# Optimization experiments

Hardware: AMD Instinct MI355X
Metric: run time of the kernel (lower is better)

Reference implementation:

```python
import jax, jax.numpy as jnp
import numpy as np

B, C, H, W = 1, 64, 128, 128
HEADS, NWIN, TOPK = 8, 16, 4
EPS = 1e-6


def dwconv(x, w, b, pad):
    # x: NCHW, w: (C,1,k,k) depthwise conv weight
    y = jax.lax.conv_general_dilated(
        x, w, (1, 1), [(pad, pad), (pad, pad)],
        dimension_numbers=('NCHW', 'OIHW', 'NCHW'),
        feature_group_count=x.shape[1])
    return y + b[None, :, None, None]


def layernorm(x, g, b):
    m = x.mean(-1, keepdims=True)
    v = ((x - m) ** 2).mean(-1, keepdims=True)
    return (x - m) * jax.lax.rsqrt(v + EPS) * g + b


def drf_attn(x, qkv_w, qkv_b, wo_w, wo_b, lepe_w, lepe_b):
    # x: (B,H,W,C) NHWC, BiFormer-style top-k routed window attention
    Bb, Hh, Ww, Cc = x.shape
    h, w = Hh // NWIN, Ww // NWIN
    hw, p2 = h * w, NWIN * NWIN
    # window partition -> (B, p2, hw, C)
    xw = x.reshape(Bb, NWIN, h, NWIN, w, Cc).transpose(0, 1, 3, 2, 4, 5).reshape(Bb, p2, hw, Cc)
    qkv = xw @ qkv_w + qkv_b                       # (B,p2,hw,3C), qk_dim == dim
    q, kv = qkv[..., :Cc], qkv[..., Cc:]
    # window-level routing: per-window mean q/k
    q_win = q.mean(2)                              # (B,p2,C)
    k_win = kv[..., :Cc].mean(2)                   # (B,p2,C)
    logits = jnp.einsum('bpc,bqc->bpq', q_win, k_win)
    _, idx = jax.lax.top_k(logits, TOPK)           # (B,p2,TOPK) int32
    # gather top-k kv windows for each query window -> (B,p2,TOPK,hw,2C)
    kv_sel = jax.vmap(lambda kvb, ib: kvb[ib])(kv, idx)
    hd = Cc // HEADS
    k_sel = kv_sel[..., :Cc].reshape(Bb, p2, TOPK * hw, HEADS, hd).transpose(0, 1, 3, 2, 4)
    v_sel = kv_sel[..., Cc:].reshape(Bb, p2, TOPK * hw, HEADS, hd).transpose(0, 1, 3, 2, 4)
    q_h = q.reshape(Bb, p2, hw, HEADS, hd).transpose(0, 1, 3, 2, 4)
    scale = Cc ** -0.5                             # qk_dim ** -0.5 as in torch module
    attn = jax.nn.softmax(jnp.einsum('bpnqd,bpnkd->bpnqk', q_h * scale, k_sel), axis=-1)
    out = jnp.einsum('bpnqk,bpnkd->bpnqd', attn, v_sel)
    out = out.transpose(0, 1, 3, 2, 4).reshape(Bb, p2, hw, Cc)
    # un-window -> (B,H,W,C)
    out = out.reshape(Bb, NWIN, NWIN, h, w, Cc).transpose(0, 1, 3, 2, 4, 5).reshape(Bb, Hh, Ww, Cc)
    # LePE: depthwise 5x5 conv on full-image v
    v_full = kv[..., Cc:].reshape(Bb, NWIN, NWIN, h, w, Cc).transpose(0, 1, 3, 2, 4, 5).reshape(Bb, Hh, Ww, Cc)
    lepe = dwconv(v_full.transpose(0, 3, 1, 2), lepe_w, lepe_b, 2).transpose(0, 2, 3, 1)
    return (out + lepe) @ wo_w + wo_b


def setup_inputs() -> dict:
    key = jax.random.key(0)
    ks = jax.random.split(key, 8)
    s = lambda k, shape: jax.random.normal(k, shape, jnp.float32) * 0.02
    return {
        'x': jax.random.normal(ks[0], (B, C, H, W), jnp.float32),
        'pos_w': s(ks[1], (C, 1, 3, 3)), 'pos_b': jnp.zeros((C,), jnp.float32),
        'norm_g': jnp.ones((C,), jnp.float32), 'norm_b': jnp.zeros((C,), jnp.float32),
        'qkv_w': s(ks[2], (C, 3 * C)), 'qkv_b': jnp.zeros((3 * C,), jnp.float32),
        'wo_w': s(ks[3], (C, C)), 'wo_b': jnp.zeros((C,), jnp.float32),
        'lepe_w': s(ks[4], (C, 1, 5, 5)), 'lepe_b': jnp.zeros((C,), jnp.float32),
        'mlp_w1': s(ks[5], (C, 4 * C)), 'mlp_b1': jnp.zeros((4 * C,), jnp.float32),
        'mlp_w2': s(ks[6], (4 * C, C)), 'mlp_b2': jnp.zeros((C,), jnp.float32),
    }


def reference(x, pos_w, pos_b, norm_g, norm_b, qkv_w, qkv_b, wo_w, wo_b,
              lepe_w, lepe_b, mlp_w1, mlp_b1, mlp_w2, mlp_b2):
    x = x + dwconv(x, pos_w, pos_b, 1)             # dwconv pos-embed (NCHW)
    x = x.transpose(0, 2, 3, 1)                    # -> NHWC
    x = x + drf_attn(layernorm(x, norm_g, norm_b), qkv_w, qkv_b, wo_w, wo_b, lepe_w, lepe_b)
    y = layernorm(x, norm_g, norm_b)               # same LayerNorm weights reused
    y = jax.nn.gelu(y @ mlp_w1 + mlp_b1, approximate=False) @ mlp_w2 + mlp_b2
    x = x + y
    return x.transpose(0, 3, 1, 2)                 # -> NCHW
```

## Files before the change

### kernel.cpp

```cpp
#include <hip/hip_runtime.h>
#include <hip/hip_bf16.h>
#include <math.h>

#define HPIX 128
#define WPIX 128
#define NPIX (HPIX*WPIX)
#define CCH 64
#define P2 256
#define HWIN 64
#define LNS 36

__device__ __forceinline__ float waveReduceSum(float v){
  #pragma unroll
  for (int m = 32; m >= 1; m >>= 1) v += __shfl_xor(v, m);
  return v;
}

__device__ __forceinline__ float gelu_exact(float h){
  return 0.5f*h*(1.f + erff(h*0.70710678118654752f));
}

__global__ void k1_posconv(const float* __restrict__ x, const float* __restrict__ pw,
                           const float* __restrict__ pb, float* __restrict__ x1){
  int tid = threadIdx.x;
  int pl = tid & 63;
  int cl = tid >> 6;
  int pix0 = (blockIdx.x & 255) * 64;
  int cg   = (blockIdx.x >> 8);
  int c = cg*4 + cl;
  int pix = pix0 + pl;
  int y = pix >> 7, xx = pix & 127;
  const float* xc = x + c*NPIX;
  float acc = pb[c];
  #pragma unroll
  for (int dy=0; dy<3; dy++){
    int yy = y+dy-1; if ((unsigned)yy >= (unsigned)HPIX) continue;
    #pragma unroll
    for (int dx=0; dx<3; dx++){
      int x2 = xx+dx-1; if ((unsigned)x2 >= (unsigned)WPIX) continue;
      acc += pw[c*9 + dy*3 + dx] * xc[yy*WPIX + x2];
    }
  }
  __shared__ float lds[4][64];
  lds[cl][pl] = xc[pix] + acc;
  __syncthreads();
  int pp = tid >> 2, cc = tid & 3;
  x1[(pix0+pp)*CCH + cg*4 + cc] = lds[cc][pp];
}

__global__ void k2_ln_qkv(const float* __restrict__ x1,
                          const float* __restrict__ g, const float* __restrict__ bb,
                          const float* __restrict__ qw, const float* __restrict__ qb,
                          float* __restrict__ qkv){
  __shared__ float lnT[64][LNS];
  int tid = threadIdx.x, w = tid >> 6, lane = tid & 63;
  int pix0 = blockIdx.x * 32;
  #pragma unroll
  for (int i=0; i<8; i++){
    int pl = w*8 + i, pix = pix0 + pl;
    float v = x1[pix*CCH + lane];
    float mean = waveReduceSum(v) * (1.f/64.f);
    float d = v - mean;
    float var = waveReduceSum(d*d) * (1.f/64.f);
    lnT[lane][pl] = d * rsqrtf(var + 1e-6f) * g[lane] + bb[lane];
  }
  __syncthreads();
  int p0 = (tid & 7) * 4;
  int cg = tid >> 3;
  int j0 = cg * 6;
  float acc[4][6];
  #pragma unroll
  for (int i=0;i<4;i++)
    #pragma unroll
    for (int j=0;j<6;j++) acc[i][j] = qb[j0+j];
  #pragma unroll 4
  for (int k=0; k<64; k++){
    float4 a = *(const float4*)&lnT[k][p0];
    const float* wr = qw + k*192 + j0;
    float2 u0 = *(const float2*)(wr);
    float2 u1 = *(const float2*)(wr+2);
    float2 u2 = *(const float2*)(wr+4);
    float av[4] = {a.x, a.y, a.z, a.w};
    #pragma unroll
    for (int i=0;i<4;i++){
      acc[i][0] += av[i]*u0.x; acc[i][1] += av[i]*u0.y;
      acc[i][2] += av[i]*u1.x; acc[i][3] += av[i]*u1.y;
      acc[i][4] += av[i]*u2.x; acc[i][5] += av[i]*u2.y;
    }
  }
  int y = pix0 >> 7;
  #pragma unroll
  for (int i=0;i<4;i++){
    int pix = pix0 + p0 + i;
    int xx = pix & 127;
    int p = (y>>3)*16 + (xx>>3);
    int r = ((y&7)<<3) + (xx&7);
    float* o = qkv + (p*HWIN + r)*192 + j0;
    *(float2*)(o)     = make_float2(acc[i][0], acc[i][1]);
    *(float2*)(o + 2) = make_float2(acc[i][2], acc[i][3]);
    *(float2*)(o + 4) = make_float2(acc[i][4], acc[i][5]);
  }
}

__global__ void k3_winmean(const float* __restrict__ qkv,
                           float* __restrict__ qwin, float* __restrict__ kwinT){
  int p = blockIdx.x;
  int tid = threadIdx.x, rq = tid >> 6, c = tid & 63;
  float sq = 0.f, sk = 0.f;
  for (int r = rq*16; r < rq*16+16; r++){
    const float* row = qkv + (p*HWIN + r)*192;
    sq += row[c];
    sk += row[64 + c];
  }
  __shared__ float s1[4][64], s2[4][64];
  s1[rq][c] = sq; s2[rq][c] = sk;
  __syncthreads();
  if (tid < 64){
    qwin[p*64 + c]   = (s1[0][c]+s1[1][c]+s1[2][c]+s1[3][c])*(1.f/64.f);
    kwinT[c*P2 + p]  = (s2[0][c]+s2[1][c]+s2[2][c]+s2[3][c])*(1.f/64.f);
  }
}

__global__ void k4_topk(const float* __restrict__ qwin, const float* __restrict__ kwinT,
                        int* __restrict__ idx){
  int p = blockIdx.x, t = threadIdx.x;
  int w = t >> 6, lane = t & 63;
  __shared__ float qs[64];
  __shared__ float lg[P2];
  __shared__ float wv[4]; __shared__ int wi[4];
  if (t < 64) qs[t] = qwin[p*64 + t];
  __syncthreads();
  float acc = 0.f;
  #pragma unroll 8
  for (int c=0; c<64; c++) acc += qs[c] * kwinT[c*P2 + t];
  lg[t] = acc;
  __syncthreads();
  for (int j=0; j<4; j++){
    float v = lg[t]; int i = t;
    #pragma unroll
    for (int m=32; m>=1; m>>=1){
      float ov = __shfl_xor(v, m); int oi = __shfl_xor(i, m);
      if (ov > v || (ov == v && oi < i)){ v = ov; i = oi; }
    }
    if (lane == 0){ wv[w] = v; wi[w] = i; }
    __syncthreads();
    if (t == 0){
      float bv = wv[0]; int bi = wi[0];
      #pragma unroll
      for (int u=1; u<4; u++)
        if (wv[u] > bv || (wv[u] == bv && wi[u] < bi)){ bv = wv[u]; bi = wi[u]; }
      idx[p*4 + j] = bi;
      lg[bi] = -1e30f;
    }
    __syncthreads();
  }
}

__global__ void k5_attn(const float* __restrict__ qkv, const int* __restrict__ idx,
                        float* __restrict__ attnout){
  int p = blockIdx.x >> 3, n = blockIdx.x & 7;
  int tid = threadIdx.x, w = tid >> 6, lane = tid & 63;
  __shared__ float Ks[256][8];
  __shared__ float Vs[256][8];
  __shared__ int wsel[4];
  __shared__ float ps[4][64][9];
  if (tid < 4) wsel[tid] = idx[p*4 + tid];
  __syncthreads();
  int cb = n*8;
  for (int u = tid; u < 512; u += 256){
    int k = u >> 1, h = u & 1;
    const float* row = qkv + (wsel[k>>6]*HWIN + (k&63))*192;
    *(float4*)&Ks[k][h*4] = *(const float4*)(row + 64  + cb + h*4);
    *(float4*)&Vs[k][h*4] = *(const float4*)(row + 128 + cb + h*4);
  }
  __syncthreads();
  const float* qrow = qkv + (p*HWIN + lane)*192 + cb;
  float q[8];
  #pragma unroll
  for (int d=0; d<8; d++) q[d] = qrow[d] * 0.125f;
  float l = 0.f, acc[8];
  #pragma unroll
  for (int d=0; d<8; d++) acc[d] = 0.f;
  #pragma unroll 4
  for (int k = w*64; k < w*64+64; k++){
    float4 ka = *(float4*)&Ks[k][0];
    float4 kb = *(float4*)&Ks[k][4];
    float s = q[0]*ka.x + q[1]*ka.y + q[2]*ka.z + q[3]*ka.w
            + q[4]*kb.x + q[5]*kb.y + q[6]*kb.z + q[7]*kb.w;
    float e = __expf(s);
    l += e;
    float4 va = *(float4*)&Vs[k][0];
    float4 vb = *(float4*)&Vs[k][4];
    acc[0]+=e*va.x; acc[1]+=e*va.y; acc[2]+=e*va.z; acc[3]+=e*va.w;
    acc[4]+=e*vb.x; acc[5]+=e*vb.y; acc[6]+=e*vb.z; acc[7]+=e*vb.w;
  }
  ps[w][lane][8] = l;
  #pragma unroll
  for (int d=0; d<8; d++) ps[w][lane][d] = acc[d];
  __syncthreads();
  if (w == 0){
    float L = 0.f, o[8];
    #pragma unroll
    for (int d=0; d<8; d++) o[d] = 0.f;
    #pragma unroll
    for (int u=0; u<4; u++){
      L += ps[u][lane][8];
      #pragma unroll
      for (int d=0; d<8; d++) o[d] += ps[u][lane][d];
    }
    float inv = 1.f / L;
    int yy = (p>>4)*8 + (lane>>3), xx = (p&15)*8 + (lane&7);
    float* orow = attnout + (yy*WPIX + xx)*CCH + cb;
    #pragma unroll
    for (int d=0; d<8; d++) orow[d] = o[d]*inv;
  }
}

__global__ void k6_lepe_wo(const float* __restrict__ attnout, const float* __restrict__ qkv,
                           const float* __restrict__ lw, const float* __restrict__ lb,
                           const float* __restrict__ ww, const float* __restrict__ wb,
                           float* __restrict__ x1){
  __shared__ float tT[64][LNS];
  int tid = threadIdx.x, w = tid >> 6, lane = tid & 63;
  int pix0 = blockIdx.x * 32;
  for (int i=0; i<8; i++){
    int pl = w*8 + i, pix = pix0 + pl;
    int y = pix >> 7, xx = pix & 127;
    float acc = lb[lane];
    #pragma unroll
    for (int dy=0; dy<5; dy++){
      int yy = y+dy-2; if ((unsigned)yy >= (unsigned)HPIX) continue;
      #pragma unroll
      for (int dx=0; dx<5; dx++){
        int x2 = xx+dx-2; if ((unsigned)x2 >= (unsigned)WPIX) continue;
        int pp = (yy>>3)*16 + (x2>>3), rr = ((yy&7)<<3) + (x2&7);
        acc += lw[lane*25 + dy*5 + dx] * qkv[(pp*HWIN + rr)*192 + 128 + lane];
      }
    }
    tT[lane][pl] = attnout[pix*CCH + lane] + acc;
  }
  __syncthreads();
  int p0 = (tid & 7) * 4;
  int cg = tid >> 3;
  int j0 = cg * 2;
  float a0[4], a1[4];
  #pragma unroll
  for (int i=0;i<4;i++){ a0[i] = wb[j0]; a1[i] = wb[j0+1]; }
  #pragma unroll 4
  for (int k=0; k<64; k++){
    float4 a = *(const float4*)&tT[k][p0];
    float2 u = *(const float2*)(ww + k*64 + j0);
    a0[0]+=a.x*u.x; a1[0]+=a.x*u.y;
    a0[1]+=a.y*u.x; a1[1]+=a.y*u.y;
    a0[2]+=a.z*u.x; a1[2]+=a.z*u.y;
    a0[3]+=a.w*u.x; a1[3]+=a.w*u.y;
  }
  #pragma unroll
  for (int i=0;i<4;i++){
    int pix = pix0 + p0 + i;
    float* xb = x1 + pix*CCH + j0;
    float2 r = *(float2*)xb;
    r.x += a0[i]; r.y += a1[i];
    *(float2*)xb = r;
  }
}

__global__ void k7_mlp_out(const float* __restrict__ x2,
                           const float* __restrict__ g, const float* __restrict__ bb,
                           const float* __restrict__ w1, const float* __restrict__ b1,
                           const float* __restrict__ w2, const float* __restrict__ b2,
                           float* __restrict__ out){
  __shared__ float lnT[64][LNS];
  __shared__ float hidT[256][LNS];
  int tid = threadIdx.x, w = tid >> 6, lane = tid & 63;
  int pix0 = blockIdx.x * 32;
  #pragma unroll
  for (int i=0; i<8; i++){
    int pl = w*8 + i, pix = pix0 + pl;
    float v = x2[pix*CCH + lane];
    float mean = waveReduceSum(v) * (1.f/64.f);
    float d = v - mean;
    float var = waveReduceSum(d*d) * (1.f/64.f);
    lnT[lane][pl] = d * rsqrtf(var + 1e-6f) * g[lane] + bb[lane];
  }
  __syncthreads();
  int p0 = (tid & 7) * 4;
  int cg = tid >> 3;
  {
    int j0 = cg * 8;
    float acc[4][8];
    #pragma unroll
    for (int i=0;i<4;i++)
      #pragma unroll
      for (int j=0;j<8;j++) acc[i][j] = b1[j0+j];
    #pragma unroll 2
    for (int k=0; k<64; k++){
      float4 a = *(const float4*)&lnT[k][p0];
      const float* wr = w1 + k*256 + j0;
      float4 u0 = *(const float4*)(wr);
      float4 u1 = *(const float4*)(wr + 4);
      float av[4] = {a.x, a.y, a.z, a.w};
      #pragma unroll
      for (int i=0;i<4;i++){
        acc[i][0]+=av[i]*u0.x; acc[i][1]+=av[i]*u0.y;
        acc[i][2]+=av[i]*u0.z; acc[i][3]+=av[i]*u0.w;
        acc[i][4]+=av[i]*u1.x; acc[i][5]+=av[i]*u1.y;
        acc[i][6]+=av[i]*u1.z; acc[i][7]+=av[i]*u1.w;
      }
    }
    #pragma unroll
    for (int j=0;j<8;j++){
      float4 hv;
      hv.x = gelu_exact(acc[0][j]);
      hv.y = gelu_exact(acc[1][j]);
      hv.z = gelu_exact(acc[2][j]);
      hv.w = gelu_exact(acc[3][j]);
      *(float4*)&hidT[j0+j][p0] = hv;
    }
  }
  __syncthreads();
  {
    int j0 = cg * 2;
    float a0[4], a1[4];
    #pragma unroll
    for (int i=0;i<4;i++){ a0[i] = b2[j0]; a1[i] = b2[j0+1]; }
    #pragma unroll 4
    for (int k=0; k<256; k++){
      float4 a = *(const float4*)&hidT[k][p0];
      float2 u = *(const float2*)(w2 + k*64 + j0);
      a0[0]+=a.x*u.x; a1[0]+=a.x*u.y;
      a0[1]+=a.y*u.x; a1[1]+=a.y*u.y;
      a0[2]+=a.z*u.x; a1[2]+=a.z*u.y;
      a0[3]+=a.w*u.x; a1[3]+=a.w*u.y;
    }
    float4 o0, o1;
    float* r0 = &o0.x; float* r1 = &o1.x;
    #pragma unroll
    for (int i=0;i<4;i++){
      int pix = pix0 + p0 + i;
      r0[i] = x2[pix*CCH + j0]     + a0[i];
      r1[i] = x2[pix*CCH + j0 + 1] + a1[i];
    }
    *(float4*)&out[j0*NPIX + pix0 + p0]     = o0;
    *(float4*)&out[(j0+1)*NPIX + pix0 + p0] = o1;
  }
}

extern "C" void kernel_launch(void* const* d_in, const int* in_sizes, int n_in,
                              void* d_out, int out_size, void* d_ws, size_t ws_size,
                              hipStream_t stream) {
  (void)in_sizes; (void)n_in; (void)out_size; (void)ws_size;
  const float* x      = (const float*)d_in[0];
  const float* pos_w  = (const float*)d_in[1];
  const float* pos_b  = (const float*)d_in[2];
  const float* norm_g = (const float*)d_in[3];
  const float* norm_b = (const float*)d_in[4];
  const float* qkv_w  = (const float*)d_in[5];
  const float* qkv_b  = (const float*)d_in[6];
  const float* wo_w   = (const float*)d_in[7];
  const float* wo_b   = (const float*)d_in[8];
  const float* lepe_w = (const float*)d_in[9];
  const float* lepe_b = (const float*)d_in[10];
  const float* mlp_w1 = (const float*)d_in[11];
  const float* mlp_b1 = (const float*)d_in[12];
  const float* mlp_w2 = (const float*)d_in[13];
  const float* mlp_b2 = (const float*)d_in[14];
  float* out = (float*)d_out;

  char* ws = (char*)d_ws;
  float* x1      = (float*)(ws);
  float* qkv     = (float*)(ws + (4u<<20));
  float* qwin    = (float*)(ws + (16u<<20));
  float* kwinT   = (float*)(ws + (16u<<20) + (64u<<10));
  int*   idx     = (int*)  (ws + (16u<<20) + (128u<<10));
  float* attnout = (float*)(ws + (17u<<20));

  hipLaunchKernelGGL(k1_posconv, dim3(4096), dim3(256), 0, stream, x, pos_w, pos_b, x1);
  hipLaunchKernelGGL(k2_ln_qkv,  dim3(512),  dim3(256), 0, stream, x1, norm_g, norm_b, qkv_w, qkv_b, qkv);
  hipLaunchKernelGGL(k3_winmean, dim3(256),  dim3(256), 0, stream, qkv, qwin, kwinT);
  hipLaunchKernelGGL(k4_topk,    dim3(256),  dim3(256), 0, stream, qwin, kwinT, idx);
  hipLaunchKernelGGL(k5_attn,    dim3(2048), dim3(256), 0, stream, qkv, idx, attnout);
  hipLaunchKernelGGL(k6_lepe_wo, dim3(512),  dim3(256), 0, stream, attnout, qkv, lepe_w, lepe_b, wo_w, wo_b, x1);
  hipLaunchKernelGGL(k7_mlp_out, dim3(512),  dim3(256), 0, stream, x1, norm_g, norm_b, mlp_w1, mlp_b1, mlp_w2, mlp_b2, out);
}
```

Baseline: 213.3 us.

## Retile QKV GEMM to 64-pixel blocks and split-K the MLP down-projection

The LN+QKV kernel now handles 64 pixels per block with 512 threads and a wider LDS tile. Its inner loop is unrolled by two k steps so more weight loads are in flight at once. In the MLP kernel, the second GEMM is split along K across the four waves, each computing a 4x8 tile, and the partials are reduced through reused shared memory before the residual add and NCHW store. The aim is more work per thread and better weight reuse in the down-projection, at the cost of an extra LDS reduction pass and less coalesced output stores.

Result: faster. 201.9 us (-5.3%).

```diff
diff --git a/kernel.cpp b/kernel.cpp
--- a/kernel.cpp
+++ b/kernel.cpp
@@ -9,6 +9,7 @@
 #define P2 256
 #define HWIN 64
 #define LNS 36
+#define LNS2 68
 
 __device__ __forceinline__ float waveReduceSum(float v){
   #pragma unroll
@@ -52,9 +53,9 @@
                           const float* __restrict__ g, const float* __restrict__ bb,
                           const float* __restrict__ qw, const float* __restrict__ qb,
                           float* __restrict__ qkv){
-  __shared__ float lnT[64][LNS];
+  __shared__ __align__(16) float lnT[64][LNS2];
   int tid = threadIdx.x, w = tid >> 6, lane = tid & 63;
-  int pix0 = blockIdx.x * 32;
+  int pix0 = blockIdx.x * 64;
   #pragma unroll
   for (int i=0; i<8; i++){
     int pl = w*8 + i, pix = pix0 + pl;
@@ -65,36 +66,47 @@
     lnT[lane][pl] = d * rsqrtf(var + 1e-6f) * g[lane] + bb[lane];
   }
   __syncthreads();
-  int p0 = (tid & 7) * 4;
-  int cg = tid >> 3;
+  int p0 = (tid & 15) * 4;
+  int cg = tid >> 4;
   int j0 = cg * 6;
   float acc[4][6];
   #pragma unroll
   for (int i=0;i<4;i++)
     #pragma unroll
     for (int j=0;j<6;j++) acc[i][j] = qb[j0+j];
-  #pragma unroll 4
-  for (int k=0; k<64; k++){
-    float4 a = *(const float4*)&lnT[k][p0];
-    const float* wr = qw + k*192 + j0;
-    float2 u0 = *(const float2*)(wr);
-    float2 u1 = *(const float2*)(wr+2);
-    float2 u2 = *(const float2*)(wr+4);
-    float av[4] = {a.x, a.y, a.z, a.w};
+  for (int k0=0; k0<64; k0+=2){
+    float4 a0 = *(const float4*)&lnT[k0][p0];
+    float4 a1 = *(const float4*)&lnT[k0+1][p0];
+    const float* wr0 = qw + k0*192 + j0;
+    const float* wr1 = wr0 + 192;
+    float2 u00 = *(const float2*)(wr0);
+    float2 u01 = *(const float2*)(wr0+2);
+    float2 u02 = *(const float2*)(wr0+4);
+    float2 u10 = *(const float2*)(wr1);
+    float2 u11 = *(const float2*)(wr1+2);
+    float2 u12 = *(const float2*)(wr1+4);
+    float a0v[4] = {a0.x,a0.y,a0.z,a0.w};
+    float a1v[4] = {a1.x,a1.y,a1.z,a1.w};
     #pragma unroll
     for (int i=0;i<4;i++){
-      acc[i][0] += av[i]*u0.x; acc[i][1] += av[i]*u0.y;
-      acc[i][2] += av[i]*u1.x; acc[i][3] += av[i]*u1.y;
-      acc[i][4] += av[i]*u2.x; acc[i][5] += av[i]*u2.y;
+      acc[i][0]+=a0v[i]*u00.x; acc[i][1]+=a0v[i]*u00.y;
+      acc[i][2]+=a0v[i]*u01.x; acc[i][3]+=a0v[i]*u01.y;
+      acc[i][4]+=a0v[i]*u02.x; acc[i][5]+=a0v[i]*u02.y;
+    }
+    #pragma unroll
+    for (int i=0;i<4;i++){
+      acc[i][0]+=a1v[i]*u10.x; acc[i][1]+=a1v[i]*u10.y;
+      acc[i][2]+=a1v[i]*u11.x; acc[i][3]+=a1v[i]*u11.y;
+      acc[i][4]+=a1v[i]*u12.x; acc[i][5]+=a1v[i]*u12.y;
     }
   }
   int y = pix0 >> 7;
+  int pb_row = (y>>3)*16, rrow = (y&7)<<3, xbase = pix0 & 127;
   #pragma unroll
   for (int i=0;i<4;i++){
-    int pix = pix0 + p0 + i;
-    int xx = pix & 127;
-    int p = (y>>3)*16 + (xx>>3);
-    int r = ((y&7)<<3) + (xx&7);
+    int xx = xbase + p0 + i;
+    int p = pb_row + (xx>>3);
+    int r = rrow + (xx&7);
     float* o = qkv + (p*HWIN + r)*192 + j0;
     *(float2*)(o)     = make_float2(acc[i][0], acc[i][1]);
     *(float2*)(o + 2) = make_float2(acc[i][2], acc[i][3]);
@@ -270,8 +282,10 @@
                            const float* __restrict__ w1, const float* __restrict__ b1,
                            const float* __restrict__ w2, const float* __restrict__ b2,
                            float* __restrict__ out){
-  __shared__ float lnT[64][LNS];
-  __shared__ float hidT[256][LNS];
+  __shared__ __align__(16) float smem[11520];
+  float (*lnT)[LNS]  = (float(*)[LNS])smem;
+  float (*hidT)[LNS] = (float(*)[LNS])(smem + 64*LNS);
+  float* red = smem;
   int tid = threadIdx.x, w = tid >> 6, lane = tid & 63;
   int pix0 = blockIdx.x * 32;
   #pragma unroll
@@ -284,28 +298,38 @@
     lnT[lane][pl] = d * rsqrtf(var + 1e-6f) * g[lane] + bb[lane];
   }
   __syncthreads();
-  int p0 = (tid & 7) * 4;
-  int cg = tid >> 3;
   {
-    int j0 = cg * 8;
+    int p0 = (tid & 7) * 4;
+    int j0 = (tid >> 3) * 8;
     float acc[4][8];
     #pragma unroll
     for (int i=0;i<4;i++)
       #pragma unroll
       for (int j=0;j<8;j++) acc[i][j] = b1[j0+j];
-    #pragma unroll 2
-    for (int k=0; k<64; k++){
-      float4 a = *(const float4*)&lnT[k][p0];
-      const float* wr = w1 + k*256 + j0;
-      float4 u0 = *(const float4*)(wr);
-      float4 u1 = *(const float4*)(wr + 4);
-      float av[4] = {a.x, a.y, a.z, a.w};
+    for (int k0=0; k0<64; k0+=2){
+      float4 a0 = *(const float4*)&lnT[k0][p0];
+      float4 a1 = *(const float4*)&lnT[k0+1][p0];
+      const float* wr0 = w1 + k0*256 + j0;
+      const float* wr1 = wr0 + 256;
+      float4 u00 = *(const float4*)(wr0);
+      float4 u01 = *(const float4*)(wr0+4);
+      float4 u10 = *(const float4*)(wr1);
+      float4 u11 = *(const float4*)(wr1+4);
+      float a0v[4] = {a0.x,a0.y,a0.z,a0.w};
+      float a1v[4] = {a1.x,a1.y,a1.z,a1.w};
       #pragma unroll
       for (int i=0;i<4;i++){
-        acc[i][0]+=av[i]*u0.x; acc[i][1]+=av[i]*u0.y;
-        acc[i][2]+=av[i]*u0.z; acc[i][3]+=av[i]*u0.w;
-        acc[i][4]+=av[i]*u1.x; acc[i][5]+=av[i]*u1.y;
-        acc[i][6]+=av[i]*u1.z; acc[i][7]+=av[i]*u1.w;
+        acc[i][0]+=a0v[i]*u00.x; acc[i][1]+=a0v[i]*u00.y;
+        acc[i][2]+=a0v[i]*u00.z; acc[i][3]+=a0v[i]*u00.w;
+        acc[i][4]+=a0v[i]*u01.x; acc[i][5]+=a0v[i]*u01.y;
+        acc[i][6]+=a0v[i]*u01.z; acc[i][7]+=a0v[i]*u01.w;
+      }
+      #pragma unroll
+      for (int i=0;i<4;i++){
+        acc[i][0]+=a1v[i]*u10.x; acc[i][1]+=a1v[i]*u10.y;
+        acc[i][2]+=a1v[i]*u10.z; acc[i][3]+=a1v[i]*u10.w;
+        acc[i][4]+=a1v[i]*u11.x; acc[i][5]+=a1v[i]*u11.y;
+        acc[i][6]+=a1v[i]*u11.z; acc[i][7]+=a1v[i]*u11.w;
       }
     }
     #pragma unroll
@@ -319,30 +343,76 @@
     }
   }
   __syncthreads();
+  float acc2[4][8];
   {
-    int j0 = cg * 2;
-    float a0[4], a1[4];
-    #pragma unroll
-    for (int i=0;i<4;i++){ a0[i] = b2[j0]; a1[i] = b2[j0+1]; }
-    #pragma unroll 4
-    for (int k=0; k<256; k++){
-      float4 a = *(const float4*)&hidT[k][p0];
-      float2 u = *(const float2*)(w2 + k*64 + j0);
-      a0[0]+=a.x*u.x; a1[0]+=a.x*u.y;
-      a0[1]+=a.y*u.x; a1[1]+=a.y*u.y;
-      a0[2]+=a.z*u.x; a1[2]+=a.z*u.y;
-      a0[3]+=a.w*u.x; a1[3]+=a.w*u.y;
-    }
-    float4 o0, o1;
-    float* r0 = &o0.x; float* r1 = &o1.x;
-    #pragma unroll
-    for (int i=0;i<4;i++){
-      int pix = pix0 + p0 + i;
-      r0[i] = x2[pix*CCH + j0]     + a0[i];
-      r1[i] = x2[pix*CCH + j0 + 1] + a1[i];
-    }
-    *(float4*)&out[j0*NPIX + pix0 + p0]     = o0;
-    *(float4*)&out[(j0+1)*NPIX + pix0 + p0] = o1;
+    int p0 = (lane & 7) * 4;
+    int c0 = (lane >> 3) * 8;
+    #pragma unroll
+    for (int i=0;i<4;i++)
+      #pragma unroll
+      for (int j=0;j<8;j++) acc2[i][j] = 0.f;
+    int kbase = w*64;
+    for (int k0=0; k0<64; k0+=2){
+      int k = kbase + k0;
+      float4 a0 = *(const float4*)&hidT[k][p0];
+      float4 a1 = *(const float4*)&hidT[k+1][p0];
+      const float* wr0 = w2 + k*64 + c0;
+      const float* wr1 = wr0 + 64;
+      float4 u00 = *(const float4*)(wr0);
+      float4 u01 = *(const float4*)(wr0+4);
+      float4 u10 = *(const float4*)(wr1);
+      float4 u11 = *(const float4*)(wr1+4);
+      float a0v[4] = {a0.x,a0.y,a0.z,a0.w};
+      float a1v[4] = {a1.x,a1.y,a1.z,a1.w};
+      #pragma unroll
+      for (int i=0;i<4;i++){
+        acc2[i][0]+=a0v[i]*u00.x; acc2[i][1]+=a0v[i]*u00.y;
+        acc2[i][2]+=a0v[i]*u00.z; acc2[i][3]+=a0v[i]*u00.w;
+        acc2[i][4]+=a0v[i]*u01.x; acc2[i][5]+=a0v[i]*u01.y;
+        acc2[i][6]+=a0v[i]*u01.z; acc2[i][7]+=a0v[i]*u01.w;
+      }
+      #pragma unroll
+      for (int i=0;i<4;i++){
+        acc2[i][0]+=a1v[i]*u10.x; acc2[i][1]+=a1v[i]*u10.y;
+        acc2[i][2]+=a1v[i]*u10.z; acc2[i][3]+=a1v[i]*u10.w;
+        acc2[i][4]+=a1v[i]*u11.x; acc2[i][5]+=a1v[i]*u11.y;
+        acc2[i][6]+=a1v[i]*u11.z; acc2[i][7]+=a1v[i]*u11.w;
+      }
+    }
+  }
+  __syncthreads();
+  #pragma unroll
+  for (int t=0; t<16; t++){
+    int s = 2*t, i = s >> 3, j = s & 7;
+    *(float2*)&red[tid*34 + s] = make_float2(acc2[i][j], acc2[i][j+1]);
+  }
+  __syncthreads();
+  {
+    int lane_r = tid & 63, ir = tid >> 6;
+    int pg = lane_r & 7, cgf = lane_r >> 3;
+    int pix = pix0 + pg*4 + ir;
+    int c0 = cgf*8;
+    float o[8];
+    #pragma unroll
+    for (int j=0;j<8;j++) o[j] = b2[c0+j];
+    #pragma unroll
+    for (int wq=0; wq<4; wq++){
+      const float* rp = &red[(wq*64 + lane_r)*34 + ir*8];
+      #pragma unroll
+      for (int j2=0;j2<4;j2++){
+        float2 pr = *(const float2*)(rp + 2*j2);
+        o[2*j2]   += pr.x;
+        o[2*j2+1] += pr.y;
+      }
+    }
+    const float* xr = x2 + pix*CCH + c0;
+    float4 r0 = *(const float4*)(xr);
+    float4 r1 = *(const float4*)(xr+4);
+    o[0]+=r0.x; o[1]+=r0.y; o[2]+=r0.z; o[3]+=r0.w;
+    o[4]+=r1.x; o[5]+=r1.y; o[6]+=r1.z; o[7]+=r1.w;
+    #pragma unroll
+    for (int j=0;j<8;j++)
+      out[(c0+j)*NPIX + pix] = o[j];
   }
 }
 
@@ -376,7 +446,7 @@
   float* attnout = (float*)(ws + (17u<<20));
 
   hipLaunchKernelGGL(k1_posconv, dim3(4096), dim3(256), 0, stream, x, pos_w, pos_b, x1);
-  hipLaunchKernelGGL(k2_ln_qkv,  dim3(512),  dim3(256), 0, stream, x1, norm_g, norm_b, qkv_w, qkv_b, qkv);
+  hipLaunchKernelGGL(k2_ln_qkv,  dim3(256),  dim3(512), 0, stream, x1, norm_g, norm_b, qkv_w, qkv_b, qkv);
   hipLaunchKernelGGL(k3_winmean, dim3(256),  dim3(256), 0, stream, qkv, qwin, kwinT);
   hipLaunchKernelGGL(k4_topk,    dim3(256),  dim3(256), 0, stream, qwin, kwinT, idx);
   hipLaunchKernelGGL(k5_attn,    dim3(2048), dim3(256), 0, stream, qkv, idx, attnout);
```
